# Kernel optimization log

Measured on AMD Instinct MI355X. Metric: run time of the kernel, lower is better.

## Reference

```python
import jax, jax.numpy as jnp
import numpy as np

F = 16384   # n_features
D = 768     # d_model
B = 2       # batch
S = 256     # seq len
C = 16      # connections per downstream feature
M = F * C   # total connections


def setup_inputs() -> dict:
    key = jax.random.key(0)
    k1, k2, k3, k4 = jax.random.split(key, 4)
    up_facts = jax.random.normal(k1, (B, S, F), dtype=jnp.float32)
    down_encoder = jax.random.normal(k2, (F, D), dtype=jnp.float32) * 0.02
    up_decoder = jax.random.normal(k3, (D, F), dtype=jnp.float32) * 0.02
    # connection_mask.nonzero() is row-major: i sorted, C targets per row
    i_indices = jnp.repeat(jnp.arange(F, dtype=jnp.int32), C)  # [M]
    j_indices = jax.random.randint(k4, (M,), 0, F, dtype=jnp.int32)  # [M]
    return {
        "up_facts": up_facts,
        "down_encoder": down_encoder,
        "up_decoder": up_decoder,
        "i_indices": i_indices,
        "j_indices": j_indices,
    }


def reference(up_facts, down_encoder, up_decoder, i_indices, j_indices):
    # up_facts: [B,S,F]; down_encoder: [F,D]; up_decoder: [D,F]
    b, s, f = up_facts.shape
    m = i_indices.shape[0]
    # per-connection virtual weight: values[m] = down_encoder[i[m]] . up_decoder[:, j[m]]
    values = jnp.einsum("md,dm->m", down_encoder[i_indices], up_decoder[:, j_indices])  # [M]
    # gather upstream feature activations and scale
    scaled = up_facts[:, :, j_indices] * values[None, None, :]  # [B,S,M]
    # scatter_add over last axis into downstream feature bins (i is constant across B,S)
    flat = scaled.reshape(b * s, m).T  # [M, B*S]
    contrib = jax.ops.segment_sum(flat, i_indices, num_segments=f)  # [F, B*S]
    return contrib.T.reshape(b, s, f)
```

## Files before the change

### kernel.cpp

```cpp
#include <hip/hip_runtime.h>
#include <hip/hip_bf16.h>

#define F_ 16384
#define D_ 768
#define C_ 16
#define BS_ 512
#define M_ (F_*C_)
#define NCHUNK 8
#define CDIM 96
#define CPB 512
#define FPB (CPB/C_)

static __device__ __forceinline__ float bf2f(unsigned short u) {
    return __uint_as_float(((unsigned int)u) << 16);
}
static __device__ __forceinline__ unsigned short f2bf(float f) {
    return __bfloat16_as_ushort(__float2bfloat16(f));
}

__global__ __launch_bounds__(256) void k_transpose_chunked(const float* __restrict__ in,
                                                           unsigned short* __restrict__ decC) {
    __shared__ float tile[64][65];
    int c4 = threadIdx.x & 15;
    int r  = threadIdx.x >> 4;
    int fbase = blockIdx.x * 64;
    int dbase = blockIdx.y * 64;
#pragma unroll
    for (int k = 0; k < 4; ++k) {
        int drow = r + k * 16;
        float4 v = *(const float4*)(in + (size_t)(dbase + drow) * F_ + fbase + c4 * 4);
        tile[drow][c4 * 4 + 0] = v.x;
        tile[drow][c4 * 4 + 1] = v.y;
        tile[drow][c4 * 4 + 2] = v.z;
        tile[drow][c4 * 4 + 3] = v.w;
    }
    __syncthreads();
    int dp = threadIdx.x & 15;
    int fr = threadIdx.x >> 4;
#pragma unroll
    for (int k = 0; k < 4; ++k) {
        int frow = fr + k * 16;
        float v0 = tile[4 * dp + 0][frow];
        float v1 = tile[4 * dp + 1][frow];
        float v2 = tile[4 * dp + 2][frow];
        float v3 = tile[4 * dp + 3][frow];
        uint2 p;
        p.x = ((unsigned int)f2bf(v1) << 16) | (unsigned int)f2bf(v0);
        p.y = ((unsigned int)f2bf(v3) << 16) | (unsigned int)f2bf(v2);
        int d  = dbase + dp * 4;
        int c  = d / CDIM;
        int dl = d - c * CDIM;
        *(uint2*)(decC + ((size_t)c * F_ + (fbase + frow)) * CDIM + dl) = p;
    }
}

#define ACC2(e, g) {                                                         \
    acc += __uint_as_float((e) << 16)        * __uint_as_float((g) << 16);   \
    acc += __uint_as_float((e) & 0xffff0000u) * __uint_as_float((g) & 0xffff0000u); }

__global__ __launch_bounds__(256, 8) void k_values_chunked(const float* __restrict__ enc,
                                                           const unsigned short* __restrict__ decC,
                                                           const int* __restrict__ jidx,
                                                           float* __restrict__ partial) {
    __shared__ unsigned short encS[FPB * CDIM];
    int chunk = blockIdx.x & 7;
    int mblk  = blockIdx.x >> 3;
    int m0 = mblk * CPB;
    int f0 = mblk * FPB;

    {
        const float* eb = enc + (size_t)f0 * D_ + chunk * CDIM;
#pragma unroll
        for (int k = 0; k < 3; ++k) {
            int idx = threadIdx.x + k * 256;
            int row = idx / 24;
            int col = idx - row * 24;
            float4 v = *(const float4*)(eb + (size_t)row * D_ + col * 4);
            uint2 p;
            p.x = ((unsigned int)f2bf(v.y) << 16) | (unsigned int)f2bf(v.x);
            p.y = ((unsigned int)f2bf(v.w) << 16) | (unsigned int)f2bf(v.z);
            *(uint2*)(encS + row * CDIM + col * 4) = p;
        }
    }
    __syncthreads();

    int lane = threadIdx.x & 63;
    int w    = threadIdx.x >> 6;
    int sub  = lane & 7;
    int cg   = lane >> 3;
    const unsigned short* db = decC + (size_t)chunk * F_ * CDIM;

    int j0 = jidx[m0 + ((0 * 4 + w) << 3) + cg];
    int j1 = jidx[m0 + ((1 * 4 + w) << 3) + cg];
    int j2 = jidx[m0 + ((2 * 4 + w) << 3) + cg];
    const char* p0 = (const char*)(db + (size_t)j0 * CDIM) + sub * 24;
    uint4 a0 = *(const uint4*)p0;
    uint2 b0 = *(const uint2*)(p0 + 16);
    const char* p1 = (const char*)(db + (size_t)j1 * CDIM) + sub * 24;
    uint4 a1 = *(const uint4*)p1;
    uint2 b1 = *(const uint2*)(p1 + 16);

#pragma unroll 4
    for (int i = 0; i < 16; ++i) {
        uint4 an; uint2 bn;
        if (i + 2 < 16) {
            const char* pn = (const char*)(db + (size_t)j2 * CDIM) + sub * 24;
            an = *(const uint4*)pn;
            bn = *(const uint2*)(pn + 16);
        }
        if (i + 3 < 16)
            j2 = jidx[m0 + (((i + 3) * 4 + w) << 3) + cg];

        int q  = i * 4 + w;
        int fl = q >> 1;
        const unsigned short* ep = encS + fl * CDIM + sub * 12;
        uint2 e0 = *(const uint2*)ep;
        uint2 e1 = *(const uint2*)(ep + 4);
        uint2 e2 = *(const uint2*)(ep + 8);
        float acc = 0.f;
        ACC2(e0.x, a0.x) ACC2(e0.y, a0.y)
        ACC2(e1.x, a0.z) ACC2(e1.y, a0.w)
        ACC2(e2.x, b0.x) ACC2(e2.y, b0.y)
        acc += __shfl_xor(acc, 1, 64);
        acc += __shfl_xor(acc, 2, 64);
        acc += __shfl_xor(acc, 4, 64);
        if (sub == 0)
            partial[(size_t)chunk * M_ + m0 + (q << 3) + cg] = acc;
        a0 = a1; b0 = b1; a1 = an; b1 = bn;
    }
}

__global__ __launch_bounds__(256) void k_pack(const float* __restrict__ partial,
                                              const int* __restrict__ jidx,
                                              unsigned int* __restrict__ packed) {
    int m = blockIdx.x * 256 + threadIdx.x;
    float s = 0.f;
#pragma unroll
    for (int c = 0; c < NCHUNK; ++c)
        s += partial[(size_t)c * M_ + m];
    packed[m] = ((unsigned int)f2bf(s) << 16) | (unsigned int)jidx[m];
}

__global__ __launch_bounds__(1024) void k_out(const float* __restrict__ up,
                                              const unsigned int* __restrict__ packed,
                                              float* __restrict__ out) {
    __shared__ unsigned int rowp[F_];
    int x    = blockIdx.x;
    int pair = ((x >> 4) << 3) | (x & 7);
    int half = (x >> 3) & 1;
    int bs0  = pair << 1;
    const float4* u0 = (const float4*)(up + (size_t)bs0 * F_);
    const float4* u1 = (const float4*)(up + (size_t)(bs0 + 1) * F_);
#pragma unroll
    for (int k = 0; k < 4; ++k) {
        int idx = threadIdx.x + k * 1024;
        float4 a = u0[idx];
        float4 b = u1[idx];
        uint4 p;
        p.x = ((unsigned int)f2bf(b.x) << 16) | (unsigned int)f2bf(a.x);
        p.y = ((unsigned int)f2bf(b.y) << 16) | (unsigned int)f2bf(a.y);
        p.z = ((unsigned int)f2bf(b.z) << 16) | (unsigned int)f2bf(a.z);
        p.w = ((unsigned int)f2bf(b.w) << 16) | (unsigned int)f2bf(a.w);
        ((uint4*)rowp)[idx] = p;
    }
    __syncthreads();
    int f0 = half << 13;
#pragma unroll 2
    for (int it = 0; it < 8; ++it) {
        int f = f0 + threadIdx.x + it * 1024;
        const uint4* sp = (const uint4*)(packed + ((size_t)f << 4));
        float a0 = 0.f, a1 = 0.f;
#pragma unroll
        for (int q = 0; q < 4; ++q) {
            uint4 wv = sp[q];
#define CONN(ww) { unsigned int p_ = rowp[(ww) & 0xffffu];                  \
                   float v_ = __uint_as_float((ww) & 0xffff0000u);          \
                   a0 += __uint_as_float(p_ << 16) * v_;                    \
                   a1 += __uint_as_float(p_ & 0xffff0000u) * v_; }
            CONN(wv.x) CONN(wv.y) CONN(wv.z) CONN(wv.w)
#undef CONN
        }
        out[(size_t)bs0 * F_ + f] = a0;
        out[(size_t)(bs0 + 1) * F_ + f] = a1;
    }
}

extern "C" void kernel_launch(void* const* d_in, const int* in_sizes, int n_in,
                              void* d_out, int out_size, void* d_ws, size_t ws_size,
                              hipStream_t stream) {
    const float* up   = (const float*)d_in[0];
    const float* enc  = (const float*)d_in[1];
    const float* dec  = (const float*)d_in[2];
    const int*   jidx = (const int*)d_in[4];
    float*       out  = (float*)d_out;

    size_t decC_bytes    = (size_t)NCHUNK * F_ * CDIM * sizeof(unsigned short);
    size_t partial_bytes = (size_t)NCHUNK * M_ * sizeof(float);
    unsigned short* decC    = (unsigned short*)d_ws;
    float*          partial = (float*)((char*)d_ws + decC_bytes);
    unsigned int*   packed  = (unsigned int*)((char*)d_ws + decC_bytes + partial_bytes);

    k_transpose_chunked<<<dim3(F_ / 64, D_ / 64), 256, 0, stream>>>(dec, decC);
    k_values_chunked<<<NCHUNK * (M_ / CPB), 256, 0, stream>>>(enc, decC, jidx, partial);
    k_pack<<<M_ / 256, 256, 0, stream>>>(partial, jidx, packed);
    k_out<<<BS_, 1024, 0, stream>>>(up, packed, out);
}
```

Baseline: 229.3 us.

## Use bf16 dot2 intrinsics, deepen prefetch, pre-pack upstream activations, retile transpose

Replaces the scalar bf16 multiply-adds with the hardware fdot2 bf16 instruction in both the values kernel and the output kernel. The values kernel's decoder-row prefetch goes from two iterations ahead to three. The fp32-to-bf16 pair packing of the upstream activations moves into a separate kernel that writes to workspace, so k_out only copies prepacked rows into shared memory, now with 512 threads per block. The transpose becomes one 96-row chunk per block. The extra kernel adds a launch and a global round-trip of the packed activations.

```diff
diff --git a/kernel.cpp b/kernel.cpp
--- a/kernel.cpp
+++ b/kernel.cpp
@@ -18,45 +18,70 @@
     return __bfloat16_as_ushort(__float2bfloat16(f));
 }
 
-__global__ __launch_bounds__(256) void k_transpose_chunked(const float* __restrict__ in,
-                                                           unsigned short* __restrict__ decC) {
-    __shared__ float tile[64][65];
-    int c4 = threadIdx.x & 15;
-    int r  = threadIdx.x >> 4;
+#if __has_builtin(__builtin_amdgcn_fdot2_f32_bf16)
+typedef __bf16 v2bf __attribute__((ext_vector_type(2)));
+static __device__ __forceinline__ float dot2bf(unsigned int e, unsigned int g, float acc) {
+    return __builtin_amdgcn_fdot2_f32_bf16(__builtin_bit_cast(v2bf, e),
+                                           __builtin_bit_cast(v2bf, g), acc, false);
+}
+#else
+static __device__ __forceinline__ float dot2bf(unsigned int e, unsigned int g, float acc) {
+    acc += __uint_as_float(e << 16) * __uint_as_float(g << 16);
+    acc += __uint_as_float(e & 0xffff0000u) * __uint_as_float(g & 0xffff0000u);
+    return acc;
+}
+#endif
+
+__global__ __launch_bounds__(256) void k_transpose96(const float* __restrict__ in,
+                                                     unsigned short* __restrict__ decC) {
+    __shared__ float tile[96][65];
     int fbase = blockIdx.x * 64;
-    int dbase = blockIdx.y * 64;
-#pragma unroll
-    for (int k = 0; k < 4; ++k) {
-        int drow = r + k * 16;
-        float4 v = *(const float4*)(in + (size_t)(dbase + drow) * F_ + fbase + c4 * 4);
-        tile[drow][c4 * 4 + 0] = v.x;
-        tile[drow][c4 * 4 + 1] = v.y;
-        tile[drow][c4 * 4 + 2] = v.z;
-        tile[drow][c4 * 4 + 3] = v.w;
+    int c     = blockIdx.y;
+    const float* src = in + (size_t)c * CDIM * F_ + fbase;
+#pragma unroll
+    for (int k = 0; k < 6; ++k) {
+        int slot = threadIdx.x + k * 256;
+        int d  = slot >> 4;
+        int f4 = slot & 15;
+        float4 v = *(const float4*)(src + (size_t)d * F_ + f4 * 4);
+        tile[d][f4 * 4 + 0] = v.x;
+        tile[d][f4 * 4 + 1] = v.y;
+        tile[d][f4 * 4 + 2] = v.z;
+        tile[d][f4 * 4 + 3] = v.w;
     }
     __syncthreads();
-    int dp = threadIdx.x & 15;
-    int fr = threadIdx.x >> 4;
-#pragma unroll
-    for (int k = 0; k < 4; ++k) {
-        int frow = fr + k * 16;
-        float v0 = tile[4 * dp + 0][frow];
-        float v1 = tile[4 * dp + 1][frow];
-        float v2 = tile[4 * dp + 2][frow];
-        float v3 = tile[4 * dp + 3][frow];
+#pragma unroll
+    for (int k = 0; k < 6; ++k) {
+        int slot = threadIdx.x + k * 256;
+        int f  = slot / 24;
+        int dg = slot - f * 24;
+        float v0 = tile[4 * dg + 0][f];
+        float v1 = tile[4 * dg + 1][f];
+        float v2 = tile[4 * dg + 2][f];
+        float v3 = tile[4 * dg + 3][f];
         uint2 p;
         p.x = ((unsigned int)f2bf(v1) << 16) | (unsigned int)f2bf(v0);
         p.y = ((unsigned int)f2bf(v3) << 16) | (unsigned int)f2bf(v2);
-        int d  = dbase + dp * 4;
-        int c  = d / CDIM;
-        int dl = d - c * CDIM;
-        *(uint2*)(decC + ((size_t)c * F_ + (fbase + frow)) * CDIM + dl) = p;
-    }
-}
-
-#define ACC2(e, g) {                                                         \
-    acc += __uint_as_float((e) << 16)        * __uint_as_float((g) << 16);   \
-    acc += __uint_as_float((e) & 0xffff0000u) * __uint_as_float((g) & 0xffff0000u); }
+        *(uint2*)(decC + ((size_t)c * F_ + fbase + f) * CDIM + 4 * dg) = p;
+    }
+}
+
+__global__ __launch_bounds__(256) void k_up_pack(const float* __restrict__ up,
+                                                 unsigned int* __restrict__ upP) {
+    size_t idx = (size_t)blockIdx.x * 256 + threadIdx.x;
+    int pair = (int)(idx >> 12);
+    int f4   = (int)(idx & 4095);
+    const float4* r0 = (const float4*)(up + (size_t)(2 * pair) * F_);
+    const float4* r1 = (const float4*)(up + (size_t)(2 * pair + 1) * F_);
+    float4 a = r0[f4];
+    float4 b = r1[f4];
+    uint4 p;
+    p.x = ((unsigned int)f2bf(b.x) << 16) | (unsigned int)f2bf(a.x);
+    p.y = ((unsigned int)f2bf(b.y) << 16) | (unsigned int)f2bf(a.y);
+    p.z = ((unsigned int)f2bf(b.z) << 16) | (unsigned int)f2bf(a.z);
+    p.w = ((unsigned int)f2bf(b.w) << 16) | (unsigned int)f2bf(a.w);
+    ((uint4*)(upP + (size_t)pair * F_))[f4] = p;
+}
 
 __global__ __launch_bounds__(256, 8) void k_values_chunked(const float* __restrict__ enc,
                                                            const unsigned short* __restrict__ decC,
@@ -90,44 +115,51 @@
     int cg   = lane >> 3;
     const unsigned short* db = decC + (size_t)chunk * F_ * CDIM;
 
-    int j0 = jidx[m0 + ((0 * 4 + w) << 3) + cg];
-    int j1 = jidx[m0 + ((1 * 4 + w) << 3) + cg];
-    int j2 = jidx[m0 + ((2 * 4 + w) << 3) + cg];
-    const char* p0 = (const char*)(db + (size_t)j0 * CDIM) + sub * 24;
-    uint4 a0 = *(const uint4*)p0;
-    uint2 b0 = *(const uint2*)(p0 + 16);
-    const char* p1 = (const char*)(db + (size_t)j1 * CDIM) + sub * 24;
-    uint4 a1 = *(const uint4*)p1;
-    uint2 b1 = *(const uint2*)(p1 + 16);
+#define JIDX(i) jidx[m0 + (((i) * 4 + w) << 3) + cg]
+    int j;
+    j = JIDX(0);
+    const char* q0 = (const char*)(db + (size_t)j * CDIM) + sub * 24;
+    uint4 a0 = *(const uint4*)q0;  uint2 b0 = *(const uint2*)(q0 + 16);
+    j = JIDX(1);
+    const char* q1 = (const char*)(db + (size_t)j * CDIM) + sub * 24;
+    uint4 a1 = *(const uint4*)q1;  uint2 b1 = *(const uint2*)(q1 + 16);
+    j = JIDX(2);
+    const char* q2 = (const char*)(db + (size_t)j * CDIM) + sub * 24;
+    uint4 a2 = *(const uint4*)q2;  uint2 b2 = *(const uint2*)(q2 + 16);
+    int jn = JIDX(3);
 
 #pragma unroll 4
     for (int i = 0; i < 16; ++i) {
-        uint4 an; uint2 bn;
-        if (i + 2 < 16) {
-            const char* pn = (const char*)(db + (size_t)j2 * CDIM) + sub * 24;
-            an = *(const uint4*)pn;
-            bn = *(const uint2*)(pn + 16);
+        uint4 na; uint2 nb;
+        if (i + 3 < 16) {
+            const char* qn = (const char*)(db + (size_t)jn * CDIM) + sub * 24;
+            na = *(const uint4*)qn;
+            nb = *(const uint2*)(qn + 16);
         }
-        if (i + 3 < 16)
-            j2 = jidx[m0 + (((i + 3) * 4 + w) << 3) + cg];
-
-        int q  = i * 4 + w;
-        int fl = q >> 1;
+        if (i + 4 < 16)
+            jn = JIDX(i + 4);
+
+        int qq = i * 4 + w;
+        int fl = qq >> 1;
         const unsigned short* ep = encS + fl * CDIM + sub * 12;
         uint2 e0 = *(const uint2*)ep;
         uint2 e1 = *(const uint2*)(ep + 4);
         uint2 e2 = *(const uint2*)(ep + 8);
         float acc = 0.f;
-        ACC2(e0.x, a0.x) ACC2(e0.y, a0.y)
-        ACC2(e1.x, a0.z) ACC2(e1.y, a0.w)
-        ACC2(e2.x, b0.x) ACC2(e2.y, b0.y)
+        acc = dot2bf(e0.x, a0.x, acc);
+        acc = dot2bf(e0.y, a0.y, acc);
+        acc = dot2bf(e1.x, a0.z, acc);
+        acc = dot2bf(e1.y, a0.w, acc);
+        acc = dot2bf(e2.x, b0.x, acc);
+        acc = dot2bf(e2.y, b0.y, acc);
         acc += __shfl_xor(acc, 1, 64);
         acc += __shfl_xor(acc, 2, 64);
         acc += __shfl_xor(acc, 4, 64);
         if (sub == 0)
-            partial[(size_t)chunk * M_ + m0 + (q << 3) + cg] = acc;
-        a0 = a1; b0 = b1; a1 = an; b1 = bn;
-    }
+            partial[(size_t)chunk * M_ + m0 + (qq << 3) + cg] = acc;
+        a0 = a1; b0 = b1; a1 = a2; b1 = b2; a2 = na; b2 = nb;
+    }
+#undef JIDX
 }
 
 __global__ __launch_bounds__(256) void k_pack(const float* __restrict__ partial,
@@ -141,44 +173,40 @@
     packed[m] = ((unsigned int)f2bf(s) << 16) | (unsigned int)jidx[m];
 }
 
-__global__ __launch_bounds__(1024) void k_out(const float* __restrict__ up,
-                                              const unsigned int* __restrict__ packed,
-                                              float* __restrict__ out) {
+__global__ __launch_bounds__(512) void k_out(const unsigned int* __restrict__ upP,
+                                             const unsigned int* __restrict__ packed,
+                                             float* __restrict__ out) {
     __shared__ unsigned int rowp[F_];
-    int x    = blockIdx.x;
-    int pair = ((x >> 4) << 3) | (x & 7);
-    int half = (x >> 3) & 1;
+    int pair = blockIdx.x >> 1;
+    int half = blockIdx.x & 1;
     int bs0  = pair << 1;
-    const float4* u0 = (const float4*)(up + (size_t)bs0 * F_);
-    const float4* u1 = (const float4*)(up + (size_t)(bs0 + 1) * F_);
-#pragma unroll
-    for (int k = 0; k < 4; ++k) {
-        int idx = threadIdx.x + k * 1024;
-        float4 a = u0[idx];
-        float4 b = u1[idx];
-        uint4 p;
-        p.x = ((unsigned int)f2bf(b.x) << 16) | (unsigned int)f2bf(a.x);
-        p.y = ((unsigned int)f2bf(b.y) << 16) | (unsigned int)f2bf(a.y);
-        p.z = ((unsigned int)f2bf(b.z) << 16) | (unsigned int)f2bf(a.z);
-        p.w = ((unsigned int)f2bf(b.w) << 16) | (unsigned int)f2bf(a.w);
-        ((uint4*)rowp)[idx] = p;
+    const uint4* src = (const uint4*)(upP + (size_t)pair * F_);
+#pragma unroll
+    for (int k = 0; k < 8; ++k) {
+        int idx = threadIdx.x + k * 512;
+        ((uint4*)rowp)[idx] = src[idx];
     }
     __syncthreads();
     int f0 = half << 13;
-#pragma unroll 2
-    for (int it = 0; it < 8; ++it) {
-        int f = f0 + threadIdx.x + it * 1024;
+#pragma unroll 4
+    for (int it = 0; it < 16; ++it) {
+        int f = f0 + threadIdx.x + it * 512;
         const uint4* sp = (const uint4*)(packed + ((size_t)f << 4));
         float a0 = 0.f, a1 = 0.f;
 #pragma unroll
         for (int q = 0; q < 4; ++q) {
             uint4 wv = sp[q];
-#define CONN(ww) { unsigned int p_ = rowp[(ww) & 0xffffu];                  \
-                   float v_ = __uint_as_float((ww) & 0xffff0000u);          \
-                   a0 += __uint_as_float(p_ << 16) * v_;                    \
-                   a1 += __uint_as_float(p_ & 0xffff0000u) * v_; }
-            CONN(wv.x) CONN(wv.y) CONN(wv.z) CONN(wv.w)
-#undef CONN
+#define CONN2(wx, wy) {                                                     \
+            unsigned int px = rowp[(wx) & 0xffffu];                         \
+            unsigned int py = rowp[(wy) & 0xffffu];                         \
+            unsigned int ev = __builtin_amdgcn_perm((wy), (wx), 0x07060302u); \
+            unsigned int g0 = __builtin_amdgcn_perm(py, px, 0x05040100u);   \
+            unsigned int g1 = __builtin_amdgcn_perm(py, px, 0x07060302u);   \
+            a0 = dot2bf(ev, g0, a0);                                        \
+            a1 = dot2bf(ev, g1, a1); }
+            CONN2(wv.x, wv.y)
+            CONN2(wv.z, wv.w)
+#undef CONN2
         }
         out[(size_t)bs0 * F_ + f] = a0;
         out[(size_t)(bs0 + 1) * F_ + f] = a1;
@@ -196,12 +224,15 @@
 
     size_t decC_bytes    = (size_t)NCHUNK * F_ * CDIM * sizeof(unsigned short);
     size_t partial_bytes = (size_t)NCHUNK * M_ * sizeof(float);
+    size_t packed_bytes  = (size_t)M_ * sizeof(unsigned int);
     unsigned short* decC    = (unsigned short*)d_ws;
     float*          partial = (float*)((char*)d_ws + decC_bytes);
     unsigned int*   packed  = (unsigned int*)((char*)d_ws + decC_bytes + partial_bytes);
-
-    k_transpose_chunked<<<dim3(F_ / 64, D_ / 64), 256, 0, stream>>>(dec, decC);
+    unsigned int*   upP     = (unsigned int*)((char*)d_ws + decC_bytes + partial_bytes + packed_bytes);
+
+    k_transpose96<<<dim3(F_ / 64, NCHUNK), 256, 0, stream>>>(dec, decC);
+    k_up_pack<<<(BS_ / 2) * (F_ / 4) / 256, 256, 0, stream>>>(up, upP);
     k_values_chunked<<<NCHUNK * (M_ / CPB), 256, 0, stream>>>(enc, decC, jidx, partial);
     k_pack<<<M_ / 256, 256, 0, stream>>>(partial, jidx, packed);
-    k_out<<<BS_, 1024, 0, stream>>>(up, packed, out);
-}
+    k_out<<<BS_, 512, 0, stream>>>(upP, packed, out);
+}
```

Measured after the change: 227.4 us. No clear change (-0.8%).
